# Optimization experiments

Measured on AMD Instinct MI355X. Metric: run time of the kernel, lower is better.

## Reference

```python
import jax, jax.numpy as jnp
import numpy as np

D = 2048
H = 16
KV = 4
DH = D // H  # 128
REP = H // KV
ROPE_BASE = 10000.0


def _rope(x, pos):
    # x: (B, h, L, Dh), pos: (L,)
    half = x.shape[-1] // 2
    inv_freq = 1.0 / (ROPE_BASE ** (jnp.arange(0, half, dtype=jnp.float32) / half))
    ang = pos.astype(jnp.float32)[:, None] * inv_freq[None, :]          # (L, half)
    cos = jnp.concatenate([jnp.cos(ang), jnp.cos(ang)], axis=-1)        # (L, Dh)
    sin = jnp.concatenate([jnp.sin(ang), jnp.sin(ang)], axis=-1)
    x1, x2 = x[..., :half], x[..., half:]
    rot = jnp.concatenate([-x2, x1], axis=-1)
    return x * cos[None, None] + rot * sin[None, None]


def setup_inputs() -> dict:
    key = jax.random.key(0)
    ks = jax.random.split(key, 5)
    s = 1.0 / np.sqrt(D)
    return {
        "x": jax.random.normal(ks[0], (2, 2048, D), dtype=jnp.float32),
        "wq": jax.random.uniform(ks[1], (H * DH, D), jnp.float32, -s, s),
        "wk": jax.random.uniform(ks[2], (KV * DH, D), jnp.float32, -s, s),
        "wv": jax.random.uniform(ks[3], (KV * DH, D), jnp.float32, -s, s),
        "wo": jax.random.uniform(ks[4], (D, H * DH), jnp.float32, -s, s),
    }


def reference(x, wq, wk, wv, wo):
    B, T, _ = x.shape
    q = (x @ wq.T).reshape(B, T, H, DH).transpose(0, 2, 1, 3)    # (B,H,T,Dh)
    k = (x @ wk.T).reshape(B, T, KV, DH).transpose(0, 2, 1, 3)   # (B,KV,T,Dh)
    v = (x @ wv.T).reshape(B, T, KV, DH).transpose(0, 2, 1, 3)
    Tc = T  # no kv cache
    pos = jnp.arange(Tc)
    q = _rope(q, pos)
    k = _rope(k, pos)
    # GQA: repeat kv heads to match query heads
    k_full = jnp.repeat(k, REP, axis=1)                          # (B,H,Tc,Dh)
    v_full = jnp.repeat(v, REP, axis=1)
    scale = 1.0 / np.sqrt(DH)
    scores = jnp.einsum('bhtd,bhsd->bhts', q, k_full) * scale    # (B,H,T,Tc)
    row = jnp.arange(T)[:, None]
    col = jnp.arange(Tc)[None, :]
    causal = col <= row + (Tc - T)
    scores = jnp.where(causal[None, None], scores, -jnp.inf)
    attn = jax.nn.softmax(scores, axis=-1)
    out = jnp.einsum('bhts,bhsd->bhtd', attn, v_full)            # (B,H,T,Dh)
    out = out.transpose(0, 2, 1, 3).reshape(B, T, H * DH)
    return out @ wo.T
```

## Files before the change

kernel.cpp:

```cpp
#include <hip/hip_runtime.h>

typedef float f32x4 __attribute__((ext_vector_type(4)));
typedef short s16x8 __attribute__((ext_vector_type(8)));
typedef unsigned short u16;

__device__ __forceinline__ u16 f2bf(float f) {
    union { float f; unsigned u; } v; v.f = f;
    return (u16)((v.u + 0x7fffu + ((v.u >> 16) & 1u)) >> 16);
}
__device__ __forceinline__ float bf2f(u16 h) {
    union { unsigned u; float f; } v; v.u = ((unsigned)h) << 16;
    return v.f;
}
__device__ __forceinline__ float fast_exp2(float x) {
#if __has_builtin(__builtin_amdgcn_exp2f)
    return __builtin_amdgcn_exp2f(x);
#else
    return exp2f(x);
#endif
}

__device__ __forceinline__ void gload_lds16(const void* g, void* l) {
    __builtin_amdgcn_global_load_lds((__attribute__((address_space(1))) void*)g,
                                     (__attribute__((address_space(3))) void*)l, 16, 0, 0);
}

__global__ __launch_bounds__(256) void cvt_all(const float* __restrict__ x,  const float* __restrict__ wq,
                                               const float* __restrict__ wk, const float* __restrict__ wv,
                                               u16* __restrict__ xb, u16* __restrict__ wqkvb) {
    int u = blockIdx.x * 256 + threadIdx.x;
    const float* src;
    u16* dst;
    if (u < 1048576) { src = x + (size_t)u * 8; dst = xb + (size_t)u * 8; }
    else {
        int w = u - 1048576;
        dst = wqkvb + (size_t)w * 8;
        if (w < 524288)      src = wq + (size_t)w * 8;
        else if (w < 655360) src = wk + (size_t)(w - 524288) * 8;
        else                 src = wv + (size_t)(w - 655360) * 8;
    }
    const float4* p = (const float4*)src;
    float4 a = p[0], b = p[1];
    s16x8 o;
    o[0] = f2bf(a.x); o[1] = f2bf(a.y); o[2] = f2bf(a.z); o[3] = f2bf(a.w);
    o[4] = f2bf(b.x); o[5] = f2bf(b.y); o[6] = f2bf(b.z); o[7] = f2bf(b.w);
    *(s16x8*)dst = o;
}

__global__ __launch_bounds__(256) void cvt_kernel(const float* __restrict__ in,
                                                  u16* __restrict__ out, int n8) {
    int i = blockIdx.x * 256 + threadIdx.x;
    if (i >= n8) return;
    const float4* p = (const float4*)(in + (size_t)i * 8);
    float4 a = p[0], b = p[1];
    s16x8 o;
    o[0] = f2bf(a.x); o[1] = f2bf(a.y); o[2] = f2bf(a.z); o[3] = f2bf(a.w);
    o[4] = f2bf(b.x); o[5] = f2bf(b.y); o[6] = f2bf(b.z); o[7] = f2bf(b.w);
    *(s16x8*)(out + (size_t)i * 8) = o;
}

__global__ __launch_bounds__(256) void norm_comb(const float* __restrict__ Opart,
                                                 const float* __restrict__ Lpart,
                                                 u16* __restrict__ ab) {
    int i = blockIdx.x * 256 + threadIdx.x;
    int c0 = (i & 63) * 8;
    int r2 = i >> 6;
    int row32 = r2 & 31;
    int r3 = r2 >> 5;
    int qsi = r3 & 31;
    int g = r3 >> 5;
    int head = c0 >> 7;
    size_t pi0 = (size_t)(g * 32 + qsi);
    size_t pi1 = (size_t)((8 + g) * 32 + qsi);
    const float* p0 = Opart + pi0 * 16384 + row32 * 512 + c0;
    const float* p1 = Opart + pi1 * 16384 + row32 * 512 + c0;
    float L0 = Lpart[pi0 * 128 + row32 * 4 + head];
    float L1 = Lpart[pi1 * 128 + row32 * 4 + head];
    float inv = 1.0f / (L0 + L1);
    int b = g >> 2, kv = g & 3;
    int token = (32 + qsi) * 32 + row32;
    u16* pd = ab + ((size_t)(b * 2048 + token) << 11) + kv * 512 + c0;
    float4 a0 = ((const float4*)p0)[0], a1 = ((const float4*)p0)[1];
    float4 b0 = ((const float4*)p1)[0], b1 = ((const float4*)p1)[1];
    s16x8 o;
    o[0] = f2bf((a0.x + b0.x) * inv); o[1] = f2bf((a0.y + b0.y) * inv);
    o[2] = f2bf((a0.z + b0.z) * inv); o[3] = f2bf((a0.w + b0.w) * inv);
    o[4] = f2bf((a1.x + b1.x) * inv); o[5] = f2bf((a1.y + b1.y) * inv);
    o[6] = f2bf((a1.z + b1.z) * inv); o[7] = f2bf((a1.w + b1.w) * inv);
    *(s16x8*)pd = o;
}

template<int OUT>
__global__ __launch_bounds__(256) void gemm128(const u16* __restrict__ A, const u16* __restrict__ B,
                                               void* __restrict__ C, void* __restrict__ Ck,
                                               void* __restrict__ Cv, int M, int N, int K) {
    __shared__ __align__(16) u16 Ald[128 * 64];
    __shared__ __align__(16) u16 Bld[128 * 64];
    const int t = threadIdx.x, wid = t >> 6, lane = t & 63;
    const int m0 = blockIdx.y * 128, n0 = blockIdx.x * 128;
    const int ml = lane & 15, quad = lane >> 4, m7 = ml & 7;
    const int wm = (wid & 1) * 64, wn = (wid >> 1) * 64;
    const int sr = lane >> 3, sc = lane & 7;

    f32x4 acc[4][4] = {};

    for (int k0 = 0; k0 < K; k0 += 64) {
        if (k0) __syncthreads();
        #pragma unroll
        for (int i = 0; i < 4; ++i) {
            int seg = wid * 4 + i;
            int r = seg * 8 + sr;
            int c = (sc ^ (r & 7)) * 8;
            gload_lds16(A + (size_t)(m0 + r) * K + k0 + c, &Ald[seg * 512]);
            gload_lds16(B + (size_t)(n0 + r) * K + k0 + c, &Bld[seg * 512]);
        }
        __syncthreads();
        #pragma unroll
        for (int kk = 0; kk < 64; kk += 32) {
            s16x8 af[4], bf[4];
            #pragma unroll
            for (int mi = 0; mi < 4; ++mi)
                af[mi] = *(const s16x8*)&Ald[(wm + mi * 16 + ml) * 64 + (((kk >> 3) + quad) ^ m7) * 8];
            #pragma unroll
            for (int ni = 0; ni < 4; ++ni)
                bf[ni] = *(const s16x8*)&Bld[(wn + ni * 16 + ml) * 64 + (((kk >> 3) + quad) ^ m7) * 8];
            #pragma unroll
            for (int mi = 0; mi < 4; ++mi)
                #pragma unroll
                for (int ni = 0; ni < 4; ++ni)
                    acc[mi][ni] = __builtin_amdgcn_mfma_f32_16x16x32_bf16(af[mi], bf[ni], acc[mi][ni], 0, 0, 0);
        }
    }
    #pragma unroll
    for (int mi = 0; mi < 4; ++mi)
        #pragma unroll
        for (int ni = 0; ni < 4; ++ni) {
            int gmb = m0 + wm + mi * 16 + quad * 4;
            int gn  = n0 + wn + ni * 16 + ml;
            if constexpr (OUT == 4) {
                if (n0 < 2048) {
                    #pragma unroll
                    for (int r = 0; r < 4; ++r)
                        ((u16*)C)[(size_t)(gmb + r) * 2048 + gn] = f2bf(acc[mi][ni][r]);
                } else if (n0 < 2560) {
                    #pragma unroll
                    for (int r = 0; r < 4; ++r)
                        ((u16*)Ck)[(size_t)(gmb + r) * 512 + (gn - 2048)] = f2bf(acc[mi][ni][r]);
                } else {
                    ushort4 v;
                    v.x = f2bf(acc[mi][ni][0]); v.y = f2bf(acc[mi][ni][1]);
                    v.z = f2bf(acc[mi][ni][2]); v.w = f2bf(acc[mi][ni][3]);
                    *(ushort4*)((u16*)Cv + (size_t)(gn - 2560) * M + gmb) = v;
                }
            } else {
                #pragma unroll
                for (int r = 0; r < 4; ++r)
                    ((float*)C)[(size_t)(gmb + r) * N + gn] = acc[mi][ni][r];
            }
        }
}

__global__ __launch_bounds__(256) void rope_kernel(u16* __restrict__ qb, u16* __restrict__ kb,
                                                   int nq, int ntot, float sq) {
    int idx = blockIdx.x * 256 + threadIdx.x;
    if (idx >= ntot) return;
    u16* base; int nheads; float scl; int id;
    if (idx < nq) { base = qb; nheads = 16; scl = sq;  id = idx; }
    else          { base = kb; nheads = 4;  scl = 1.f; id = idx - nq; }
    int i = id & 63;
    int rest = id >> 6;
    int hh = rest % nheads;
    int tok = rest / nheads;
    int tpos = tok & 2047;
    u16* row = base + (size_t)tok * nheads * 128 + hh * 128;
    float x1 = bf2f(row[i]);
    float x2 = bf2f(row[i + 64]);
    float inv = expf(-(float)i * 0.14391156731570787f);
    float ang = (float)tpos * inv;
    float s, c;
    sincosf(ang, &s, &c);
    row[i]      = f2bf((x1 * c - x2 * s) * scl);
    row[i + 64] = f2bf((x2 * c + x1 * s) * scl);
}

__global__ __launch_bounds__(256, 4) void attn_kernel(const u16* __restrict__ Q, const u16* __restrict__ Kb,
                                                      const u16* __restrict__ Vt, u16* __restrict__ O) {
    __shared__ __align__(16) u16 Klds[64 * 128];
    __shared__ __align__(16) u16 Vlds[128 * 64];
    __shared__ __align__(16) u16 Plds[4][16 * 64];
    const int t = threadIdx.x, wslot = t >> 6, lane = t & 63;
    const int kv = blockIdx.y, b = blockIdx.z;
    const int g = kv + 4 * b;
    const int bx = blockIdx.x;
    int qt;
    switch ((g >> 1) & 3) {
        case 0:  qt = bx; break;
        case 1:  qt = 127 - bx; break;
        case 2:  qt = (bx + 64) & 127; break;
        default: qt = (63 - bx) & 127; break;
    }
    const int h = kv * 4 + wslot;
    const int ml = lane & 15, quad = lane >> 4, m7 = ml & 7;
    const int t0 = qt * 16;
    const int n = (qt >> 2) + 1;

    s16x8 qf[4];
    {
        const u16* qp = Q + ((size_t)(b * 2048 + t0 + ml) * 2048 + h * 128);
        #pragma unroll
        for (int kc = 0; kc < 4; ++kc)
            qf[kc] = *(const s16x8*)(qp + kc * 32 + quad * 8);
    }

    s16x8 ones;
    #pragma unroll
    for (int j = 0; j < 8; ++j) ones[j] = (short)0x3F80;

    f32x4 Oa[8] = {};
    f32x4 L = {};

    for (int it = 0; it < n; ++it) {
        const int s0 = it * 64;
        if (it) __syncthreads();
        #pragma unroll
        for (int i = 0; i < 4; ++i) {
            int seg = wslot * 4 + i;
            int kr = seg * 4 + (lane >> 4);
            int kc = ((lane & 15) ^ (kr & 7)) * 8;
            gload_lds16(Kb + (size_t)(b * 2048 + s0 + kr) * 512 + kv * 128 + kc, &Klds[seg * 512]);
            int vr = seg * 8 + (lane >> 3);
            int vc = ((lane & 7) ^ (vr & 7)) * 8;
            gload_lds16(Vt + (size_t)(kv * 128 + vr) * 4096 + b * 2048 + s0 + vc, &Vlds[seg * 512]);
        }
        __syncthreads();

        f32x4 S[4] = {};
        #pragma unroll
        for (int kc = 0; kc < 4; ++kc)
            #pragma unroll
            for (int ti = 0; ti < 4; ++ti) {
                s16x8 kf = *(const s16x8*)&Klds[(ti * 16 + ml) * 128 + ((kc * 4 + quad) ^ m7) * 8];
                S[ti] = __builtin_amdgcn_mfma_f32_16x16x32_bf16(qf[kc], kf, S[ti], 0, 0, 0);
            }

        {
            u16* pl = &Plds[wslot][0];
            const bool diag = (it == n - 1);
            #pragma unroll
            for (int r = 0; r < 4; ++r) {
                int qr = t0 + quad * 4 + r;
                int row = quad * 4 + r;
                #pragma unroll
                for (int ti = 0; ti < 4; ++ti) {
                    float e = fast_exp2(S[ti][r]);
                    if (diag && (s0 + ti * 16 + ml > qr)) e = 0.f;
                    union { float f; unsigned u; } cv; cv.f = e;
                    pl[row * 64 + (((ti * 2 + (ml >> 3)) ^ (row & 7)) * 8) + (ml & 7)] = (u16)(cv.u >> 16);
                }
            }
        }
        asm volatile("s_waitcnt lgkmcnt(0)" ::: "memory");
        s16x8 pf[2];
        pf[0] = *(const s16x8*)&Plds[wslot][ml * 64 + ((quad)     ^ m7) * 8];
        pf[1] = *(const s16x8*)&Plds[wslot][ml * 64 + ((4 + quad) ^ m7) * 8];
        asm volatile("s_waitcnt lgkmcnt(0)" ::: "memory");

        #pragma unroll
        for (int c = 0; c < 2; ++c) {
            #pragma unroll
            for (int nt = 0; nt < 8; ++nt) {
                s16x8 vf = *(const s16x8*)&Vlds[(nt * 16 + ml) * 64 + ((c * 4 + quad) ^ m7) * 8];
                Oa[nt] = __builtin_amdgcn_mfma_f32_16x16x32_bf16(pf[c], vf, Oa[nt], 0, 0, 0);
            }
            L = __builtin_amdgcn_mfma_f32_16x16x32_bf16(pf[c], ones, L, 0, 0, 0);
        }
    }

    #pragma unroll
    for (int nt = 0; nt < 8; ++nt)
        #pragma unroll
        for (int r = 0; r < 4; ++r) {
            int col = h * 128 + nt * 16 + ml;
            O[(size_t)(b * 2048 + t0 + quad * 4 + r) * 2048 + col] = f2bf(Oa[nt][r] / L[r]);
        }
}

__global__ __launch_bounds__(256, 3) void attn_pair(const u16* __restrict__ Q, const u16* __restrict__ Kb,
                                                    const u16* __restrict__ Vt, u16* __restrict__ O,
                                                    float* __restrict__ Opart, float* __restrict__ Lpart) {
    __shared__ __align__(16) u16 Klds[64 * 128];
    __shared__ __align__(16) u16 Vlds[128 * 64];
    __shared__ __align__(16) u16 Plds[4][2][16 * 64];
    const int t = threadIdx.x, wslot = t >> 6, lane = t & 63;
    const int bid = blockIdx.x;
    const int g = bid & 7, idx = bid >> 3;
    const int kv = g & 3, b = g >> 2;

    int qs, it0, it1, n, hsel = 0;
    bool partial;
    if (idx < 64) {
        int p = idx >> 1; hsel = idx & 1;
        qs = 63 - p; n = (qs >> 1) + 1;
        int nh = n >> 1;
        it0 = hsel ? nh : 0;
        it1 = hsel ? n : nh;
        partial = true;
    } else {
        qs = 95 - idx; n = (qs >> 1) + 1;
        it0 = 0; it1 = n;
        partial = false;
    }

    const int h = kv * 4 + wslot;
    const int ml = lane & 15, quad = lane >> 4, m7 = ml & 7;
    const int t0a = qs * 32, t0b = qs * 32 + 16;

    s16x8 qfA[4], qfB[4];
    {
        const u16* qpA = Q + ((size_t)(b * 2048 + t0a + ml) * 2048 + h * 128);
        const u16* qpB = Q + ((size_t)(b * 2048 + t0b + ml) * 2048 + h * 128);
        #pragma unroll
        for (int kc = 0; kc < 4; ++kc) {
            qfA[kc] = *(const s16x8*)(qpA + kc * 32 + quad * 8);
            qfB[kc] = *(const s16x8*)(qpB + kc * 32 + quad * 8);
        }
    }

    s16x8 ones;
    #pragma unroll
    for (int j = 0; j < 8; ++j) ones[j] = (short)0x3F80;

    f32x4 OA[8] = {}, OB[8] = {};
    f32x4 LA = {}, LB = {};

    for (int it = it0; it < it1; ++it) {
        const int s0 = it * 64;
        if (it != it0) __syncthreads();
        #pragma unroll
        for (int i = 0; i < 4; ++i) {
            int seg = wslot * 4 + i;
            int kr = seg * 4 + (lane >> 4);
            int kc = ((lane & 15) ^ (kr & 7)) * 8;
            gload_lds16(Kb + (size_t)(b * 2048 + s0 + kr) * 512 + kv * 128 + kc, &Klds[seg * 512]);
            int vr = seg * 8 + (lane >> 3);
            int vc = ((lane & 7) ^ (vr & 7)) * 8;
            gload_lds16(Vt + (size_t)(kv * 128 + vr) * 4096 + b * 2048 + s0 + vc, &Vlds[seg * 512]);
        }
        __syncthreads();

        f32x4 Sa[4] = {}, Sb[4] = {};
        #pragma unroll
        for (int kc = 0; kc < 4; ++kc)
            #pragma unroll
            for (int ti = 0; ti < 4; ++ti) {
                s16x8 kf = *(const s16x8*)&Klds[(ti * 16 + ml) * 128 + ((kc * 4 + quad) ^ m7) * 8];
                Sa[ti] = __builtin_amdgcn_mfma_f32_16x16x32_bf16(qfA[kc], kf, Sa[ti], 0, 0, 0);
                Sb[ti] = __builtin_amdgcn_mfma_f32_16x16x32_bf16(qfB[kc], kf, Sb[ti], 0, 0, 0);
            }

        const bool diag = (it == n - 1);
        auto do_soft = [&](f32x4* S, int t0, int pslot) {
            u16* pl = &Plds[wslot][pslot][0];
            #pragma unroll
            for (int r = 0; r < 4; ++r) {
                int qr = t0 + quad * 4 + r;
                int row = quad * 4 + r;
                #pragma unroll
                for (int ti = 0; ti < 4; ++ti) {
                    float e = fast_exp2(S[ti][r]);
                    if (diag && (s0 + ti * 16 + ml > qr)) e = 0.f;
                    union { float f; unsigned u; } cv; cv.f = e;
                    pl[row * 64 + (((ti * 2 + (ml >> 3)) ^ (row & 7)) * 8) + (ml & 7)] = (u16)(cv.u >> 16);
                }
            }
        };
        do_soft(Sa, t0a, 0);
        do_soft(Sb, t0b, 1);
        asm volatile("s_waitcnt lgkmcnt(0)" ::: "memory");
        s16x8 pfA[2], pfB[2];
        pfA[0] = *(const s16x8*)&Plds[wslot][0][ml * 64 + ((quad)     ^ m7) * 8];
        pfA[1] = *(const s16x8*)&Plds[wslot][0][ml * 64 + ((4 + quad) ^ m7) * 8];
        pfB[0] = *(const s16x8*)&Plds[wslot][1][ml * 64 + ((quad)     ^ m7) * 8];
        pfB[1] = *(const s16x8*)&Plds[wslot][1][ml * 64 + ((4 + quad) ^ m7) * 8];
        asm volatile("s_waitcnt lgkmcnt(0)" ::: "memory");

        #pragma unroll
        for (int c = 0; c < 2; ++c) {
            #pragma unroll
            for (int nt = 0; nt < 8; ++nt) {
                s16x8 vf = *(const s16x8*)&Vlds[(nt * 16 + ml) * 64 + ((c * 4 + quad) ^ m7) * 8];
                OA[nt] = __builtin_amdgcn_mfma_f32_16x16x32_bf16(pfA[c], vf, OA[nt], 0, 0, 0);
                OB[nt] = __builtin_amdgcn_mfma_f32_16x16x32_bf16(pfB[c], vf, OB[nt], 0, 0, 0);
            }
            LA = __builtin_amdgcn_mfma_f32_16x16x32_bf16(pfA[c], ones, LA, 0, 0, 0);
            LB = __builtin_amdgcn_mfma_f32_16x16x32_bf16(pfB[c], ones, LB, 0, 0, 0);
        }
    }

    if (!partial) {
        #pragma unroll
        for (int nt = 0; nt < 8; ++nt)
            #pragma unroll
            for (int r = 0; r < 4; ++r) {
                int col = h * 128 + nt * 16 + ml;
                O[(size_t)(b * 2048 + t0a + quad * 4 + r) * 2048 + col] = f2bf(OA[nt][r] / LA[r]);
                O[(size_t)(b * 2048 + t0b + quad * 4 + r) * 2048 + col] = f2bf(OB[nt][r] / LB[r]);
            }
    } else {
        const size_t pi = (size_t)((hsel * 8 + g) * 32 + (qs - 32));
        float* Ob = Opart + pi * 16384;
        float* Lb = Lpart + pi * 128;
        #pragma unroll
        for (int nt = 0; nt < 8; ++nt)
            #pragma unroll
            for (int r = 0; r < 4; ++r) {
                int c = wslot * 128 + nt * 16 + ml;
                Ob[(quad * 4 + r) * 512 + c]        = OA[nt][r];
                Ob[(16 + quad * 4 + r) * 512 + c]   = OB[nt][r];
            }
        if (ml == 0) {
            #pragma unroll
            for (int r = 0; r < 4; ++r) {
                Lb[(quad * 4 + r) * 4 + wslot]      = LA[r];
                Lb[(16 + quad * 4 + r) * 4 + wslot] = LB[r];
            }
        }
    }
}

extern "C" void kernel_launch(void* const* d_in, const int* in_sizes, int n_in,
                              void* d_out, int out_size, void* d_ws, size_t ws_size,
                              hipStream_t stream) {
    const float* x  = (const float*)d_in[0];
    const float* wq = (const float*)d_in[1];
    const float* wk = (const float*)d_in[2];
    const float* wv = (const float*)d_in[3];
    const float* wo = (const float*)d_in[4];
    float* out = (float*)d_out;
    char* ws = (char*)d_ws;

    const size_t MB = 1024 * 1024;
    u16* xb    = (u16*)(ws);
    u16* qb    = (u16*)(ws + 16 * MB);
    u16* kb    = (u16*)(ws + 32 * MB);
    u16* vtb   = (u16*)(ws + 36 * MB);
    u16* wqkvb = (u16*)(ws + 40 * MB);
    u16* ab    = xb;
    u16* wob   = wqkvb;

    const bool split = ws_size >= 53 * MB;

    cvt_all<<<7168, 256, 0, stream>>>(x, wq, wk, wv, xb, wqkvb);

    gemm128<4><<<dim3(24, 32), 256, 0, stream>>>(xb, wqkvb, qb, kb, vtb, 4096, 3072, 2048);

    cvt_kernel<<<2048, 256, 0, stream>>>(wo, wob, 524288);

    rope_kernel<<<20480, 256, 0, stream>>>(qb, kb, 4194304, 5242880, 0.12751743f);

    if (split) {
        float* Opart = out;
        float* Lpart = (float*)(ws + 52 * MB);
        attn_pair<<<768, 256, 0, stream>>>(qb, kb, vtb, ab, Opart, Lpart);
        norm_comb<<<2048, 256, 0, stream>>>(Opart, Lpart, ab);
    } else {
        attn_kernel<<<dim3(128, 4, 2), 256, 0, stream>>>(qb, kb, vtb, ab);
    }

    gemm128<1><<<dim3(16, 32), 256, 0, stream>>>(ab, wob, out, nullptr, nullptr, 4096, 2048, 2048);
}
```

Measured before the change: 351.9 us.

## Split long causal attention query tiles three ways and mid tiles two ways

Reworks the attention work split. The longest query tiles (qs 48–63) are now divided into three KV-range partials, tiles 24–47 into two, and the shortest ones stay whole. This raises the grid from 768 to 960 blocks to even out per-block work and cut the tail. The partials spill into the output buffer plus a new 16 MB workspace region, and the combine kernel now sums a variable number of partials. It costs more partial-write traffic and needs a larger workspace, falling back to the unsplit path if that space is missing.

```diff
diff --git a/kernel.cpp b/kernel.cpp
--- a/kernel.cpp
+++ b/kernel.cpp
@@ -59,34 +59,43 @@
     *(s16x8*)(out + (size_t)i * 8) = o;
 }
 
-__global__ __launch_bounds__(256) void norm_comb(const float* __restrict__ Opart,
+__global__ __launch_bounds__(256) void norm_comb(const float* __restrict__ OpA,
+                                                 const float* __restrict__ OpB,
                                                  const float* __restrict__ Lpart,
                                                  u16* __restrict__ ab) {
     int i = blockIdx.x * 256 + threadIdx.x;
     int c0 = (i & 63) * 8;
-    int r2 = i >> 6;
-    int row32 = r2 & 31;
-    int r3 = r2 >> 5;
-    int qsi = r3 & 31;
-    int g = r3 >> 5;
+    int r = i >> 6;
+    int row32 = r & 31;
+    int r2 = r >> 5;
+    int qsi = r2 % 40;
+    int g = r2 / 40;
+    int qs = 24 + qsi;
     int head = c0 >> 7;
-    size_t pi0 = (size_t)(g * 32 + qsi);
-    size_t pi1 = (size_t)((8 + g) * 32 + qsi);
-    const float* p0 = Opart + pi0 * 16384 + row32 * 512 + c0;
-    const float* p1 = Opart + pi1 * 16384 + row32 * 512 + c0;
-    float L0 = Lpart[pi0 * 128 + row32 * 4 + head];
-    float L1 = Lpart[pi1 * 128 + row32 * 4 + head];
-    float inv = 1.0f / (L0 + L1);
+    int base, np;
+    if (qs < 48) { base = (qs - 24) * 2;      np = 2; }
+    else         { base = 48 + (qs - 48) * 3; np = 3; }
+    float4 s0 = {0.f, 0.f, 0.f, 0.f}, s1 = {0.f, 0.f, 0.f, 0.f};
+    float Ls = 0.f;
+    for (int p = 0; p < np; ++p) {
+        int slot = g * 96 + base + p;
+        const float* Ob = (slot < 512) ? (OpA + (size_t)slot * 16384)
+                                       : (OpB + (size_t)(slot - 512) * 16384);
+        const float* po = Ob + row32 * 512 + c0;
+        float4 a = ((const float4*)po)[0], b = ((const float4*)po)[1];
+        s0.x += a.x; s0.y += a.y; s0.z += a.z; s0.w += a.w;
+        s1.x += b.x; s1.y += b.y; s1.z += b.z; s1.w += b.w;
+        Ls += Lpart[(size_t)slot * 128 + row32 * 4 + head];
+    }
+    float inv = 1.0f / Ls;
     int b = g >> 2, kv = g & 3;
-    int token = (32 + qsi) * 32 + row32;
+    int token = qs * 32 + row32;
     u16* pd = ab + ((size_t)(b * 2048 + token) << 11) + kv * 512 + c0;
-    float4 a0 = ((const float4*)p0)[0], a1 = ((const float4*)p0)[1];
-    float4 b0 = ((const float4*)p1)[0], b1 = ((const float4*)p1)[1];
     s16x8 o;
-    o[0] = f2bf((a0.x + b0.x) * inv); o[1] = f2bf((a0.y + b0.y) * inv);
-    o[2] = f2bf((a0.z + b0.z) * inv); o[3] = f2bf((a0.w + b0.w) * inv);
-    o[4] = f2bf((a1.x + b1.x) * inv); o[5] = f2bf((a1.y + b1.y) * inv);
-    o[6] = f2bf((a1.z + b1.z) * inv); o[7] = f2bf((a1.w + b1.w) * inv);
+    o[0] = f2bf(s0.x * inv); o[1] = f2bf(s0.y * inv);
+    o[2] = f2bf(s0.z * inv); o[3] = f2bf(s0.w * inv);
+    o[4] = f2bf(s1.x * inv); o[5] = f2bf(s1.y * inv);
+    o[6] = f2bf(s1.z * inv); o[7] = f2bf(s1.w * inv);
     *(s16x8*)pd = o;
 }
 
@@ -287,7 +296,8 @@
 
 __global__ __launch_bounds__(256, 3) void attn_pair(const u16* __restrict__ Q, const u16* __restrict__ Kb,
                                                     const u16* __restrict__ Vt, u16* __restrict__ O,
-                                                    float* __restrict__ Opart, float* __restrict__ Lpart) {
+                                                    float* __restrict__ OpA, float* __restrict__ OpB,
+                                                    float* __restrict__ Lpart) {
     __shared__ __align__(16) u16 Klds[64 * 128];
     __shared__ __align__(16) u16 Vlds[128 * 64];
     __shared__ __align__(16) u16 Plds[4][2][16 * 64];
@@ -296,19 +306,26 @@
     const int g = bid & 7, idx = bid >> 3;
     const int kv = g & 3, b = g >> 2;
 
-    int qs, it0, it1, n, hsel = 0;
+    int qs, it0, it1, n, psel = 0;
     bool partial;
-    if (idx < 64) {
-        int p = idx >> 1; hsel = idx & 1;
-        qs = 63 - p; n = (qs >> 1) + 1;
+    if (idx < 12) {
+        qs = 23 - idx; n = (qs >> 1) + 1; it0 = 0; it1 = n; partial = false;
+    } else if (idx < 60) {
+        int p = (idx - 12) >> 1; psel = (idx - 12) & 1;
+        qs = 47 - p; n = (qs >> 1) + 1;
         int nh = n >> 1;
-        it0 = hsel ? nh : 0;
-        it1 = hsel ? n : nh;
+        it0 = psel ? nh : 0;
+        it1 = psel ? n : nh;
+        partial = true;
+    } else if (idx < 108) {
+        int q3 = (idx - 60) / 3; psel = (idx - 60) % 3;
+        qs = 63 - q3; n = (qs >> 1) + 1;
+        int a = n / 3, b2 = (2 * n) / 3;
+        it0 = (psel == 0) ? 0 : ((psel == 1) ? a : b2);
+        it1 = (psel == 0) ? a : ((psel == 1) ? b2 : n);
         partial = true;
     } else {
-        qs = 95 - idx; n = (qs >> 1) + 1;
-        it0 = 0; it1 = n;
-        partial = false;
+        qs = 119 - idx; n = (qs >> 1) + 1; it0 = 0; it1 = n; partial = false;
     }
 
     const int h = kv * 4 + wslot;
@@ -407,16 +424,18 @@
                 O[(size_t)(b * 2048 + t0b + quad * 4 + r) * 2048 + col] = f2bf(OB[nt][r] / LB[r]);
             }
     } else {
-        const size_t pi = (size_t)((hsel * 8 + g) * 32 + (qs - 32));
-        float* Ob = Opart + pi * 16384;
-        float* Lb = Lpart + pi * 128;
+        int base = (qs < 48) ? (qs - 24) * 2 : 48 + (qs - 48) * 3;
+        int slot = g * 96 + base + psel;
+        float* Ob = (slot < 512) ? (OpA + (size_t)slot * 16384)
+                                 : (OpB + (size_t)(slot - 512) * 16384);
+        float* Lb = Lpart + (size_t)slot * 128;
         #pragma unroll
         for (int nt = 0; nt < 8; ++nt)
             #pragma unroll
             for (int r = 0; r < 4; ++r) {
                 int c = wslot * 128 + nt * 16 + ml;
-                Ob[(quad * 4 + r) * 512 + c]        = OA[nt][r];
-                Ob[(16 + quad * 4 + r) * 512 + c]   = OB[nt][r];
+                Ob[(quad * 4 + r) * 512 + c]      = OA[nt][r];
+                Ob[(16 + quad * 4 + r) * 512 + c] = OB[nt][r];
             }
         if (ml == 0) {
             #pragma unroll
@@ -448,7 +467,7 @@
     u16* ab    = xb;
     u16* wob   = wqkvb;
 
-    const bool split = ws_size >= 53 * MB;
+    const bool split = ws_size >= 69 * MB;
 
     cvt_all<<<7168, 256, 0, stream>>>(x, wq, wk, wv, xb, wqkvb);
 
@@ -459,10 +478,11 @@
     rope_kernel<<<20480, 256, 0, stream>>>(qb, kb, 4194304, 5242880, 0.12751743f);
 
     if (split) {
-        float* Opart = out;
-        float* Lpart = (float*)(ws + 52 * MB);
-        attn_pair<<<768, 256, 0, stream>>>(qb, kb, vtb, ab, Opart, Lpart);
-        norm_comb<<<2048, 256, 0, stream>>>(Opart, Lpart, ab);
+        float* OpA   = out;
+        float* OpB   = (float*)(ws + 52 * MB);
+        float* Lpart = (float*)(ws + 68 * MB);
+        attn_pair<<<960, 256, 0, stream>>>(qb, kb, vtb, ab, OpA, OpB, Lpart);
+        norm_comb<<<2560, 256, 0, stream>>>(OpA, OpB, Lpart, ab);
     } else {
         attn_kernel<<<dim3(128, 4, 2), 256, 0, stream>>>(qb, kb, vtb, ab);
     }
```

Result: slower. 360.7 us (+2.5%).
